# Kernel tuning notes

Hardware: AMD Instinct MI355X
Metric: run time of the kernel (lower is better)

## Reference

```python
import jax, jax.numpy as jnp
import numpy as np

S = 4096  # source_sequence_size
Q = 4096  # query_sequence_size
E = 2048  # embedding_size
D = 2048  # output_embedding_size


def setup_inputs() -> dict:
    key = jax.random.key(0)
    ks = jax.random.split(key, 9)
    s = 1.0 / np.sqrt(E)
    return {
        "key": jax.random.normal(ks[0], (S, E), jnp.float32),
        "value": jax.random.normal(ks[1], (S, E), jnp.float32),
        "query": jax.random.normal(ks[2], (Q, E), jnp.float32),
        "Wk": jax.random.normal(ks[3], (D, E), jnp.float32) * s,
        "bk": jax.random.normal(ks[4], (D,), jnp.float32) * 0.01,
        "Wq": jax.random.normal(ks[5], (D, E), jnp.float32) * s,
        "bq": jax.random.normal(ks[6], (D,), jnp.float32) * 0.01,
        "Wv": jax.random.normal(ks[7], (D, E), jnp.float32) * s,
        "bv": jax.random.normal(ks[8], (D,), jnp.float32) * 0.01,
    }


def reference(key, value, query, Wk, bk, Wq, bq, Wv, bv):
    # Linear projections (nn.Linear: x @ W.T + b)
    k = key @ Wk.T + bk      # [S, D]
    v = value @ Wv.T + bv    # [S, D]
    q = query @ Wq.T + bq    # [Q, D]
    # Per-query-token attention scores over all source tokens (schema BOTH),
    # then weighted sum over value rows -- vectorized form of the per-token
    # apply_attention_scores loop.
    scale = 1.0 / jnp.sqrt(jnp.asarray(D, q.dtype))
    scores = jax.nn.softmax(jnp.einsum("qd,sd->qs", q, k) * scale, axis=-1)  # [Q, S]
    return jnp.einsum("qs,sd->qd", scores, v)  # [Q, D]
```

## Files before the change

kernel.cpp:

```cpp
#include <hip/hip_runtime.h>

#define S_SEQ 4096
#define Q_SEQ 4096
#define E_DIM 2048
#define D_DIM 2048

typedef __bf16 bf16;
typedef __bf16 bf16x4 __attribute__((ext_vector_type(4)));
typedef __bf16 bf16x8 __attribute__((ext_vector_type(8)));
typedef float f32x4 __attribute__((ext_vector_type(4)));

__global__ __launch_bounds__(256) void cast6(
    const float* __restrict__ i0, const float* __restrict__ i1,
    const float* __restrict__ i2, const float* __restrict__ i3,
    const float* __restrict__ i4, const float* __restrict__ i5,
    bf16* __restrict__ o0, bf16* __restrict__ o1, bf16* __restrict__ o2,
    bf16* __restrict__ o3, bf16* __restrict__ o4, bf16* __restrict__ o5) {
  const float* in;
  bf16* out;
  int n4;
  switch (blockIdx.y) {
    case 0: in = i0; out = o0; n4 = (S_SEQ * E_DIM) / 4; break;
    case 1: in = i1; out = o1; n4 = (S_SEQ * E_DIM) / 4; break;
    case 2: in = i2; out = o2; n4 = (S_SEQ * E_DIM) / 4; break;
    case 3: in = i3; out = o3; n4 = (D_DIM * E_DIM) / 4; break;
    case 4: in = i4; out = o4; n4 = (D_DIM * E_DIM) / 4; break;
    default: in = i5; out = o5; n4 = (D_DIM * E_DIM) / 4; break;
  }
  int i = blockIdx.x * 256 + threadIdx.x;
  if (i < n4) {
    float4 v = reinterpret_cast<const float4*>(in)[i];
    bf16x4 o;
    o[0] = (bf16)v.x; o[1] = (bf16)v.y; o[2] = (bf16)v.z; o[3] = (bf16)v.w;
    *reinterpret_cast<bf16x4*>(out + 4 * (size_t)i) = o;
  }
}

__device__ __forceinline__ void async_copy16(const bf16* g, bf16* l) {
  __builtin_amdgcn_global_load_lds(
      (const __attribute__((address_space(1))) void*)g,
      (__attribute__((address_space(3))) void*)l, 16, 0, 0);
}

__device__ __forceinline__ void xcd_remap32(int id, int nt, int& m, int& n) {
  int xcd = id & 7;
  int lid = id >> 3;
  m = (xcd & 3) * 8 + (lid & 7);
  n = (xcd >> 2) * (nt >> 1) + (lid >> 3);
}
__device__ __forceinline__ void xcd_remap16(int id, int nt, int& m, int& n) {
  int xcd = id & 7;
  int lid = id >> 3;
  m = (xcd & 3) * 4 + (lid & 3);
  n = (xcd >> 2) * (nt >> 1) + (lid >> 2);
}

template <int EPI>
__device__ __forceinline__ void gemm_body_sb(
    const bf16* __restrict__ A, int lda,
    const bf16* __restrict__ B, int ldb,
    void* __restrict__ C, int ldc,
    const float* __restrict__ aux, float scale, int K, int mBase, int nBase) {
  __shared__ __align__(16) bf16 Als[128 * 64];
  __shared__ __align__(16) bf16 Bls[128 * 64];

  const int tid  = threadIdx.x;
  const int wave = tid >> 6;
  const int lane = tid & 63;
  const int quad = lane >> 4;
  const int lrow = lane & 15;
  const int wRow = (wave >> 1) * 64;
  const int wCol = (wave & 1) * 64;

  f32x4 acc[4][4];
#pragma unroll
  for (int i = 0; i < 4; ++i)
#pragma unroll
    for (int j = 0; j < 4; ++j) {
      f32x4 z = {0.f, 0.f, 0.f, 0.f};
      acc[i][j] = z;
    }

  for (int k0 = 0; k0 < K; k0 += 64) {
#pragma unroll
    for (int c = 0; c < 4; ++c) {
      int chunk = c * 256 + tid;
      int row = chunk >> 3;
      int kc = (chunk & 7) ^ (row & 7);
      const bf16* g = A + (size_t)(mBase + row) * lda + k0 + kc * 8;
      async_copy16(g, Als + (size_t)(c * 256 + wave * 64) * 8);
    }
#pragma unroll
    for (int c = 0; c < 4; ++c) {
      int chunk = c * 256 + tid;
      int row = chunk >> 3;
      int kc = (chunk & 7) ^ (row & 7);
      const bf16* g = B + (size_t)(nBase + row) * ldb + k0 + kc * 8;
      async_copy16(g, Bls + (size_t)(c * 256 + wave * 64) * 8);
    }
    __syncthreads();

#pragma unroll
    for (int kk = 0; kk < 2; ++kk) {
      bf16x8 af[4], bfr[4];
#pragma unroll
      for (int i = 0; i < 4; ++i) {
        int r = wRow + i * 16 + lrow;
        int slot = (kk * 4 + quad) ^ (r & 7);
        af[i] = *(const bf16x8*)(Als + (size_t)r * 64 + slot * 8);
      }
#pragma unroll
      for (int j = 0; j < 4; ++j) {
        int r = wCol + j * 16 + lrow;
        int slot = (kk * 4 + quad) ^ (r & 7);
        bfr[j] = *(const bf16x8*)(Bls + (size_t)r * 64 + slot * 8);
      }
#pragma unroll
      for (int i = 0; i < 4; ++i)
#pragma unroll
        for (int j = 0; j < 4; ++j)
          acc[i][j] = __builtin_amdgcn_mfma_f32_16x16x32_bf16(af[i], bfr[j], acc[i][j], 0, 0, 0);
    }
    __syncthreads();
  }

  float rinv[4][4];
  if (EPI == 2) {
#pragma unroll
    for (int i = 0; i < 4; ++i)
#pragma unroll
      for (int r = 0; r < 4; ++r)
        rinv[i][r] = aux[mBase + wRow + i * 16 + quad * 4 + r];
  }
#pragma unroll
  for (int j = 0; j < 4; ++j) {
    const int cn = nBase + wCol + j * 16 + lrow;
    float bj = 0.f;
    if (EPI == 0) bj = aux[cn];
#pragma unroll
    for (int i = 0; i < 4; ++i) {
      const int rbase = mBase + wRow + i * 16 + quad * 4;
#pragma unroll
      for (int r = 0; r < 4; ++r) {
        if (EPI == 0)
          ((bf16*)C)[(size_t)(rbase + r) * ldc + cn] = (bf16)(acc[i][j][r] + bj);
        else if (EPI == 1)
          ((bf16*)C)[(size_t)(rbase + r) * ldc + cn] =
              (bf16)__expf(acc[i][j][r] * scale);
        else
          ((float*)C)[(size_t)(rbase + r) * ldc + cn] = acc[i][j][r] * rinv[i][r];
      }
    }
  }
}

__device__ __forceinline__ void stage_half(const bf16* __restrict__ G, int ld,
                                           int grow0, int k0, bf16* lds,
                                           int wave, int lane) {
#pragma unroll
  for (int s = 0; s < 2; ++s) {
    int c = (wave * 2 + s) * 64 + lane;
    int row = c >> 3;
    int kc = (c & 7) ^ (row & 7);
    const bf16* g = G + (size_t)(grow0 + row) * ld + k0 + kc * 8;
    async_copy16(g, lds + (size_t)(wave * 2 + s) * 512);
  }
}

#define BARRIER __builtin_amdgcn_s_barrier()
#define LGKM0 asm volatile("s_waitcnt lgkmcnt(0)" ::: "memory")
#define VMCNT2 asm volatile("s_waitcnt vmcnt(2)" ::: "memory")
#define VMCNT0 asm volatile("s_waitcnt vmcnt(0)" ::: "memory")

#define RD_A(buf, IP)                                                         \
  _Pragma("unroll") for (int ii = 0; ii < 2; ++ii)                            \
  _Pragma("unroll") for (int kk = 0; kk < 2; ++kk)                            \
      aR[ii][kk] = *(const bf16x8*)(&Als[buf][(size_t)(wRow + ((IP)*2 + ii) * 16 + lrow) * 64 + slotk[kk] * 8]);

#define RD_B(buf, JP, dst)                                                    \
  _Pragma("unroll") for (int jj = 0; jj < 2; ++jj)                            \
  _Pragma("unroll") for (int kk = 0; kk < 2; ++kk)                            \
      dst[jj][kk] = *(const bf16x8*)(&Bls[buf][(size_t)(wCol + ((JP)*2 + jj) * 16 + lrow) * 64 + slotk[kk] * 8]);

#define MMA16(IP)                                                              \
  __builtin_amdgcn_s_setprio(1);                                               \
  _Pragma("unroll") for (int jj = 0; jj < 2; ++jj)                             \
  _Pragma("unroll") for (int ii = 0; ii < 2; ++ii)                             \
  _Pragma("unroll") for (int kk = 0; kk < 2; ++kk)                             \
      acc[(IP)*2 + ii][jj] = __builtin_amdgcn_mfma_f32_16x16x32_bf16(          \
          aR[ii][kk], b0[jj][kk], acc[(IP)*2 + ii][jj], 0, 0, 0);              \
  _Pragma("unroll") for (int jj = 0; jj < 2; ++jj)                             \
  _Pragma("unroll") for (int ii = 0; ii < 2; ++ii)                             \
  _Pragma("unroll") for (int kk = 0; kk < 2; ++kk)                             \
      acc[(IP)*2 + ii][2 + jj] = __builtin_amdgcn_mfma_f32_16x16x32_bf16(      \
          aR[ii][kk], b1[jj][kk], acc[(IP)*2 + ii][2 + jj], 0, 0, 0);          \
  __builtin_amdgcn_s_setprio(0)

template <int EPI>
__device__ __forceinline__ void gemm_body_4ph(
    const bf16* __restrict__ A, int lda,
    const bf16* __restrict__ B, int ldb,
    void* __restrict__ C, int ldc,
    const float* __restrict__ aux, float scale, int K, int mBase, int nBase,
    float* __restrict__ psum) {
  __shared__ __align__(16) bf16 Als[2][256 * 64];
  __shared__ __align__(16) bf16 Bls[2][128 * 64];

  const int tid  = threadIdx.x;
  const int wave = tid >> 6;
  const int lane = tid & 63;
  const int quad = lane >> 4;
  const int lrow = lane & 15;
  const int wRow = (wave >> 1) * 64;
  const int wCol = (wave & 1) * 64;
  const int slotk[2] = {quad ^ (lrow & 7), (4 + quad) ^ (lrow & 7)};

  f32x4 acc[4][4];
#pragma unroll
  for (int i = 0; i < 4; ++i)
#pragma unroll
    for (int j = 0; j < 4; ++j) {
      f32x4 z = {0.f, 0.f, 0.f, 0.f};
      acc[i][j] = z;
    }

  bf16x8 aR[2][2], b0[2][2], b1[2][2];

  stage_half(B, ldb, nBase, 0, &Bls[0][0], wave, lane);
  stage_half(A, lda, mBase, 0, &Als[0][0], wave, lane);
  stage_half(A, lda, mBase + 128, 0, &Als[0][128 * 64], wave, lane);
  stage_half(B, ldb, nBase, 64, &Bls[1][0], wave, lane);
  VMCNT2;
  BARRIER;

  const int NI = K >> 7;
#pragma unroll 1
  for (int i = 0; i < NI; ++i) {
    const bool nl = (i + 1 < NI);
    const int kb = i * 128;
    RD_A(0, 0);
    RD_B(0, 0, b0);
    RD_B(0, 1, b1);
    stage_half(A, lda, mBase, kb + 64, &Als[1][0], wave, lane);
    stage_half(A, lda, mBase + 128, kb + 64, &Als[1][128 * 64], wave, lane);
    BARRIER; LGKM0; MMA16(0); BARRIER;
    RD_A(0, 1);
    if (nl) {
      stage_half(B, ldb, nBase, kb + 128, &Bls[0][0], wave, lane);
      VMCNT2;
    } else {
      VMCNT0;
    }
    BARRIER; LGKM0; MMA16(1); BARRIER;
    RD_A(1, 0);
    RD_B(1, 0, b0);
    RD_B(1, 1, b1);
    if (nl) {
      stage_half(A, lda, mBase, kb + 128, &Als[0][0], wave, lane);
      stage_half(A, lda, mBase + 128, kb + 128, &Als[0][128 * 64], wave, lane);
    }
    BARRIER; LGKM0; MMA16(0); BARRIER;
    RD_A(1, 1);
    if (nl) {
      stage_half(B, ldb, nBase, kb + 192, &Bls[1][0], wave, lane);
      VMCNT2;
    }
    BARRIER; LGKM0; MMA16(1); BARRIER;
  }

  float rinv[4][4];
  if (EPI == 2) {
#pragma unroll
    for (int i = 0; i < 4; ++i)
#pragma unroll
      for (int r = 0; r < 4; ++r)
        rinv[i][r] = aux[mBase + wRow + i * 16 + quad * 4 + r];
  }
  float sp[4][4];
  if (EPI == 1) {
#pragma unroll
    for (int i = 0; i < 4; ++i)
#pragma unroll
      for (int r = 0; r < 4; ++r) sp[i][r] = 0.f;
  }
#pragma unroll
  for (int j = 0; j < 4; ++j) {
    const int cn = nBase + wCol + j * 16 + lrow;
    float bj = 0.f;
    if (EPI == 0) bj = aux[cn];
#pragma unroll
    for (int i = 0; i < 4; ++i) {
      const int rbase = mBase + wRow + i * 16 + quad * 4;
#pragma unroll
      for (int r = 0; r < 4; ++r) {
        if (EPI == 0) {
          ((bf16*)C)[(size_t)(rbase + r) * ldc + cn] = (bf16)(acc[i][j][r] + bj);
        } else if (EPI == 1) {
          bf16 eb = (bf16)__expf(acc[i][j][r] * scale);
          ((bf16*)C)[(size_t)(rbase + r) * ldc + cn] = eb;
          sp[i][r] += (float)eb;
        } else {
          ((float*)C)[(size_t)(rbase + r) * ldc + cn] = acc[i][j][r] * rinv[i][r];
        }
      }
    }
  }
  if (EPI == 1) {
#pragma unroll
    for (int i = 0; i < 4; ++i)
#pragma unroll
      for (int r = 0; r < 4; ++r) {
#pragma unroll
        for (int off = 1; off < 16; off <<= 1)
          sp[i][r] += __shfl_xor(sp[i][r], off, 64);
      }
    if (lrow == 0) {
      const int col64 = (nBase + wCol) >> 6;
#pragma unroll
      for (int i = 0; i < 4; ++i) {
        const int rbase = mBase + wRow + i * 16 + quad * 4;
#pragma unroll
        for (int r = 0; r < 4; ++r)
          psum[(size_t)(rbase + r) * 64 + col64] = sp[i][r];
      }
    }
  }
}

__global__ __launch_bounds__(512, 2) void qk_gemm(
    const bf16* __restrict__ A, const bf16* __restrict__ B,
    bf16* __restrict__ E, float scale,
    const bf16* __restrict__ v, bf16* __restrict__ vT,
    float* __restrict__ psum) {
  if (blockIdx.x >= 512) {
    __shared__ bf16 ttile[64][66];
    const int t = threadIdx.x;
    const int col = t & 63;
    const int r8 = t >> 6;
    const int base = (blockIdx.x - 512) * 4;
#pragma unroll 1
    for (int t4 = 0; t4 < 4; ++t4) {
      const int id = base + t4;
      const int c0 = (id & 31) * 64;
      const int r0 = (id >> 5) * 64;
#pragma unroll
      for (int i = 0; i < 8; ++i) {
        int rr = i * 8 + r8;
        ttile[rr][col] = v[(size_t)(r0 + rr) * D_DIM + c0 + col];
      }
      __syncthreads();
#pragma unroll
      for (int i = 0; i < 8; ++i) {
        int rr = i * 8 + r8;
        vT[(size_t)(c0 + rr) * S_SEQ + r0 + col] = ttile[col][rr];
      }
      __syncthreads();
    }
    return;
  }
  int m, n;
  xcd_remap16(blockIdx.x, 32, m, n);
  gemm_body_4ph<1>(A, D_DIM, B, D_DIM, (void*)E, S_SEQ, nullptr, scale, D_DIM,
                   m * 256, n * 128, psum);
}

__global__ __launch_bounds__(512, 2) void pv_gemm(
    const bf16* __restrict__ E, const bf16* __restrict__ vT,
    float* __restrict__ out, const float* __restrict__ inv) {
  int m, n;
  xcd_remap16(blockIdx.x, 16, m, n);
  gemm_body_4ph<2>(E, S_SEQ, vT, S_SEQ, (void*)out, D_DIM, inv, 0.f, S_SEQ,
                   m * 256, n * 128, nullptr);
}

__global__ __launch_bounds__(256, 2) void proj_gemm(
    const bf16* __restrict__ xk, const bf16* __restrict__ xq,
    const bf16* __restrict__ xv,
    const bf16* __restrict__ Wk, const bf16* __restrict__ Wq,
    const bf16* __restrict__ Wv,
    const float* __restrict__ bk, const float* __restrict__ bq,
    const float* __restrict__ bv,
    bf16* __restrict__ ok, bf16* __restrict__ oq, bf16* __restrict__ ov) {
  const bf16 *A, *W;
  const float* b;
  bf16* o;
  switch (blockIdx.z) {
    case 0: A = xk; W = Wk; b = bk; o = ok; break;
    case 1: A = xq; W = Wq; b = bq; o = oq; break;
    default: A = xv; W = Wv; b = bv; o = ov; break;
  }
  int m, n;
  xcd_remap32(blockIdx.x, 16, m, n);
  gemm_body_sb<0>(A, E_DIM, W, E_DIM, (void*)o, D_DIM, b, 0.f, E_DIM,
                  m * 128, n * 128);
}

__global__ __launch_bounds__(256) void rowsum2(
    const float* __restrict__ psum, float* __restrict__ inv) {
  const int r = blockIdx.x * 256 + threadIdx.x;
  const f32x4* p = (const f32x4*)(psum + (size_t)r * 64);
  float s = 0.f;
#pragma unroll
  for (int i = 0; i < 16; ++i) {
    f32x4 v = p[i];
    s += v[0] + v[1] + v[2] + v[3];
  }
  inv[r] = 1.0f / s;
}

extern "C" void kernel_launch(void* const* d_in, const int* in_sizes, int n_in,
                              void* d_out, int out_size, void* d_ws, size_t ws_size,
                              hipStream_t stream) {
  const float* key   = (const float*)d_in[0];
  const float* value = (const float*)d_in[1];
  const float* query = (const float*)d_in[2];
  const float* Wk = (const float*)d_in[3];
  const float* bk = (const float*)d_in[4];
  const float* Wq = (const float*)d_in[5];
  const float* bq = (const float*)d_in[6];
  const float* Wv = (const float*)d_in[7];
  const float* bv = (const float*)d_in[8];

  const size_t MB = 1ull << 20;
  char* ws = (char*)d_ws;
  bf16* key_bf   = (bf16*)(ws + 0 * MB);
  bf16* value_bf = (bf16*)(ws + 16 * MB);
  bf16* query_bf = (bf16*)(ws + 32 * MB);
  bf16* Wk_bf    = (bf16*)(ws + 48 * MB);
  bf16* Wq_bf    = (bf16*)(ws + 56 * MB);
  bf16* Wv_bf    = (bf16*)(ws + 64 * MB);
  bf16* k_bf     = (bf16*)(ws + 72 * MB);
  bf16* q_bf     = (bf16*)(ws + 88 * MB);
  bf16* v_bf     = (bf16*)(ws + 104 * MB);
  bf16* vT_bf    = (bf16*)(ws + 120 * MB);
  bf16* E        = (bf16*)(ws + 0 * MB);
  float* psum    = (float*)(ws + 34 * MB);
  float* inv     = (float*)(ws + 35 * MB);

  dim3 blk(256);
  dim3 blk512(512);

  cast6<<<dim3(8192, 6), blk, 0, stream>>>(
      key, value, query, Wk, Wq, Wv,
      key_bf, value_bf, query_bf, Wk_bf, Wq_bf, Wv_bf);

  proj_gemm<<<dim3(512, 1, 3), blk, 0, stream>>>(
      key_bf, query_bf, value_bf, Wk_bf, Wq_bf, Wv_bf, bk, bq, bv,
      k_bf, q_bf, v_bf);

  const float scale = 0.022097086912079608f;
  qk_gemm<<<dim3(1024), blk512, 0, stream>>>(q_bf, k_bf, E, scale,
                                             v_bf, vT_bf, psum);

  rowsum2<<<dim3(16), blk, 0, stream>>>(psum, inv);

  pv_gemm<<<dim3(256), blk512, 0, stream>>>(E, vT_bf, (float*)d_out, inv);
}
```

Measured before the change: 419.3 us.

## Replace 4-phase double-buffered attention GEMMs with single-buffer 256-thread GEMM

The QK and PV GEMMs drop the 512-thread, 4-phase, double-buffered LDS pipeline with priority hints. They now use a simpler 256-thread body: one LDS buffer, a 64-deep K step, and an 8x4 MFMA tile per wave. The V transpose path is adapted to 256 threads. The fp32-to-bf16 cast kernel becomes a grid-stride loop over 512 blocks instead of 8192. This cuts register pressure, barriers and launch overhead, but the global loads no longer overlap with MFMA work, which risks exposing memory latency.

```diff
diff --git a/kernel.cpp b/kernel.cpp
--- a/kernel.cpp
+++ b/kernel.cpp
@@ -27,8 +27,9 @@
     case 4: in = i4; out = o4; n4 = (D_DIM * E_DIM) / 4; break;
     default: in = i5; out = o5; n4 = (D_DIM * E_DIM) / 4; break;
   }
-  int i = blockIdx.x * 256 + threadIdx.x;
-  if (i < n4) {
+  const int stride = 512 * 256;
+#pragma unroll 2
+  for (int i = blockIdx.x * 256 + threadIdx.x; i < n4; i += stride) {
     float4 v = reinterpret_cast<const float4*>(in)[i];
     bf16x4 o;
     o[0] = (bf16)v.x; o[1] = (bf16)v.y; o[2] = (bf16)v.z; o[3] = (bf16)v.w;
@@ -124,14 +125,6 @@
     __syncthreads();
   }
 
-  float rinv[4][4];
-  if (EPI == 2) {
-#pragma unroll
-    for (int i = 0; i < 4; ++i)
-#pragma unroll
-      for (int r = 0; r < 4; ++r)
-        rinv[i][r] = aux[mBase + wRow + i * 16 + quad * 4 + r];
-  }
 #pragma unroll
   for (int j = 0; j < 4; ++j) {
     const int cn = nBase + wCol + j * 16 + lrow;
@@ -144,158 +137,105 @@
       for (int r = 0; r < 4; ++r) {
         if (EPI == 0)
           ((bf16*)C)[(size_t)(rbase + r) * ldc + cn] = (bf16)(acc[i][j][r] + bj);
-        else if (EPI == 1)
-          ((bf16*)C)[(size_t)(rbase + r) * ldc + cn] =
-              (bf16)__expf(acc[i][j][r] * scale);
-        else
-          ((float*)C)[(size_t)(rbase + r) * ldc + cn] = acc[i][j][r] * rinv[i][r];
-      }
-    }
-  }
-}
-
-__device__ __forceinline__ void stage_half(const bf16* __restrict__ G, int ld,
-                                           int grow0, int k0, bf16* lds,
-                                           int wave, int lane) {
-#pragma unroll
-  for (int s = 0; s < 2; ++s) {
-    int c = (wave * 2 + s) * 64 + lane;
-    int row = c >> 3;
-    int kc = (c & 7) ^ (row & 7);
-    const bf16* g = G + (size_t)(grow0 + row) * ld + k0 + kc * 8;
-    async_copy16(g, lds + (size_t)(wave * 2 + s) * 512);
-  }
-}
-
-#define BARRIER __builtin_amdgcn_s_barrier()
-#define LGKM0 asm volatile("s_waitcnt lgkmcnt(0)" ::: "memory")
-#define VMCNT2 asm volatile("s_waitcnt vmcnt(2)" ::: "memory")
-#define VMCNT0 asm volatile("s_waitcnt vmcnt(0)" ::: "memory")
-
-#define RD_A(buf, IP)                                                         \
-  _Pragma("unroll") for (int ii = 0; ii < 2; ++ii)                            \
-  _Pragma("unroll") for (int kk = 0; kk < 2; ++kk)                            \
-      aR[ii][kk] = *(const bf16x8*)(&Als[buf][(size_t)(wRow + ((IP)*2 + ii) * 16 + lrow) * 64 + slotk[kk] * 8]);
-
-#define RD_B(buf, JP, dst)                                                    \
-  _Pragma("unroll") for (int jj = 0; jj < 2; ++jj)                            \
-  _Pragma("unroll") for (int kk = 0; kk < 2; ++kk)                            \
-      dst[jj][kk] = *(const bf16x8*)(&Bls[buf][(size_t)(wCol + ((JP)*2 + jj) * 16 + lrow) * 64 + slotk[kk] * 8]);
-
-#define MMA16(IP)                                                              \
-  __builtin_amdgcn_s_setprio(1);                                               \
-  _Pragma("unroll") for (int jj = 0; jj < 2; ++jj)                             \
-  _Pragma("unroll") for (int ii = 0; ii < 2; ++ii)                             \
-  _Pragma("unroll") for (int kk = 0; kk < 2; ++kk)                             \
-      acc[(IP)*2 + ii][jj] = __builtin_amdgcn_mfma_f32_16x16x32_bf16(          \
-          aR[ii][kk], b0[jj][kk], acc[(IP)*2 + ii][jj], 0, 0, 0);              \
-  _Pragma("unroll") for (int jj = 0; jj < 2; ++jj)                             \
-  _Pragma("unroll") for (int ii = 0; ii < 2; ++ii)                             \
-  _Pragma("unroll") for (int kk = 0; kk < 2; ++kk)                             \
-      acc[(IP)*2 + ii][2 + jj] = __builtin_amdgcn_mfma_f32_16x16x32_bf16(      \
-          aR[ii][kk], b1[jj][kk], acc[(IP)*2 + ii][2 + jj], 0, 0, 0);          \
-  __builtin_amdgcn_s_setprio(0)
+      }
+    }
+  }
+}
 
 template <int EPI>
-__device__ __forceinline__ void gemm_body_4ph(
+__device__ __forceinline__ void gemm_body_c(
     const bf16* __restrict__ A, int lda,
     const bf16* __restrict__ B, int ldb,
     void* __restrict__ C, int ldc,
     const float* __restrict__ aux, float scale, int K, int mBase, int nBase,
     float* __restrict__ psum) {
-  __shared__ __align__(16) bf16 Als[2][256 * 64];
-  __shared__ __align__(16) bf16 Bls[2][128 * 64];
+  __shared__ __align__(16) bf16 Als[256 * 64];
+  __shared__ __align__(16) bf16 Bls[128 * 64];
 
   const int tid  = threadIdx.x;
   const int wave = tid >> 6;
   const int lane = tid & 63;
   const int quad = lane >> 4;
   const int lrow = lane & 15;
-  const int wRow = (wave >> 1) * 64;
+  const int wRow = (wave >> 1) * 128;
   const int wCol = (wave & 1) * 64;
-  const int slotk[2] = {quad ^ (lrow & 7), (4 + quad) ^ (lrow & 7)};
-
-  f32x4 acc[4][4];
-#pragma unroll
-  for (int i = 0; i < 4; ++i)
+
+  f32x4 acc[8][4];
+#pragma unroll
+  for (int i = 0; i < 8; ++i)
 #pragma unroll
     for (int j = 0; j < 4; ++j) {
       f32x4 z = {0.f, 0.f, 0.f, 0.f};
       acc[i][j] = z;
     }
 
-  bf16x8 aR[2][2], b0[2][2], b1[2][2];
-
-  stage_half(B, ldb, nBase, 0, &Bls[0][0], wave, lane);
-  stage_half(A, lda, mBase, 0, &Als[0][0], wave, lane);
-  stage_half(A, lda, mBase + 128, 0, &Als[0][128 * 64], wave, lane);
-  stage_half(B, ldb, nBase, 64, &Bls[1][0], wave, lane);
-  VMCNT2;
-  BARRIER;
-
-  const int NI = K >> 7;
-#pragma unroll 1
-  for (int i = 0; i < NI; ++i) {
-    const bool nl = (i + 1 < NI);
-    const int kb = i * 128;
-    RD_A(0, 0);
-    RD_B(0, 0, b0);
-    RD_B(0, 1, b1);
-    stage_half(A, lda, mBase, kb + 64, &Als[1][0], wave, lane);
-    stage_half(A, lda, mBase + 128, kb + 64, &Als[1][128 * 64], wave, lane);
-    BARRIER; LGKM0; MMA16(0); BARRIER;
-    RD_A(0, 1);
-    if (nl) {
-      stage_half(B, ldb, nBase, kb + 128, &Bls[0][0], wave, lane);
-      VMCNT2;
-    } else {
-      VMCNT0;
-    }
-    BARRIER; LGKM0; MMA16(1); BARRIER;
-    RD_A(1, 0);
-    RD_B(1, 0, b0);
-    RD_B(1, 1, b1);
-    if (nl) {
-      stage_half(A, lda, mBase, kb + 128, &Als[0][0], wave, lane);
-      stage_half(A, lda, mBase + 128, kb + 128, &Als[0][128 * 64], wave, lane);
-    }
-    BARRIER; LGKM0; MMA16(0); BARRIER;
-    RD_A(1, 1);
-    if (nl) {
-      stage_half(B, ldb, nBase, kb + 192, &Bls[1][0], wave, lane);
-      VMCNT2;
-    }
-    BARRIER; LGKM0; MMA16(1); BARRIER;
-  }
-
-  float rinv[4][4];
+  for (int k0 = 0; k0 < K; k0 += 64) {
+#pragma unroll
+    for (int c = 0; c < 8; ++c) {
+      int chunk = c * 256 + tid;
+      int row = chunk >> 3;
+      int kc = (chunk & 7) ^ (row & 7);
+      const bf16* g = A + (size_t)(mBase + row) * lda + k0 + kc * 8;
+      async_copy16(g, Als + (size_t)(c * 256 + wave * 64) * 8);
+    }
+#pragma unroll
+    for (int c = 0; c < 4; ++c) {
+      int chunk = c * 256 + tid;
+      int row = chunk >> 3;
+      int kc = (chunk & 7) ^ (row & 7);
+      const bf16* g = B + (size_t)(nBase + row) * ldb + k0 + kc * 8;
+      async_copy16(g, Bls + (size_t)(c * 256 + wave * 64) * 8);
+    }
+    __syncthreads();
+
+#pragma unroll
+    for (int kk = 0; kk < 2; ++kk) {
+      bf16x8 af[8], bfr[4];
+#pragma unroll
+      for (int i = 0; i < 8; ++i) {
+        int r = wRow + i * 16 + lrow;
+        int slot = (kk * 4 + quad) ^ (r & 7);
+        af[i] = *(const bf16x8*)(Als + (size_t)r * 64 + slot * 8);
+      }
+#pragma unroll
+      for (int j = 0; j < 4; ++j) {
+        int r = wCol + j * 16 + lrow;
+        int slot = (kk * 4 + quad) ^ (r & 7);
+        bfr[j] = *(const bf16x8*)(Bls + (size_t)r * 64 + slot * 8);
+      }
+#pragma unroll
+      for (int i = 0; i < 8; ++i)
+#pragma unroll
+        for (int j = 0; j < 4; ++j)
+          acc[i][j] = __builtin_amdgcn_mfma_f32_16x16x32_bf16(af[i], bfr[j], acc[i][j], 0, 0, 0);
+    }
+    __syncthreads();
+  }
+
+  float rinv[8][4];
   if (EPI == 2) {
 #pragma unroll
-    for (int i = 0; i < 4; ++i)
+    for (int i = 0; i < 8; ++i)
 #pragma unroll
       for (int r = 0; r < 4; ++r)
         rinv[i][r] = aux[mBase + wRow + i * 16 + quad * 4 + r];
   }
-  float sp[4][4];
+  float sp[8][4];
   if (EPI == 1) {
 #pragma unroll
-    for (int i = 0; i < 4; ++i)
+    for (int i = 0; i < 8; ++i)
 #pragma unroll
       for (int r = 0; r < 4; ++r) sp[i][r] = 0.f;
   }
 #pragma unroll
   for (int j = 0; j < 4; ++j) {
     const int cn = nBase + wCol + j * 16 + lrow;
-    float bj = 0.f;
-    if (EPI == 0) bj = aux[cn];
-#pragma unroll
-    for (int i = 0; i < 4; ++i) {
+#pragma unroll
+    for (int i = 0; i < 8; ++i) {
       const int rbase = mBase + wRow + i * 16 + quad * 4;
 #pragma unroll
       for (int r = 0; r < 4; ++r) {
-        if (EPI == 0) {
-          ((bf16*)C)[(size_t)(rbase + r) * ldc + cn] = (bf16)(acc[i][j][r] + bj);
-        } else if (EPI == 1) {
+        if (EPI == 1) {
           bf16 eb = (bf16)__expf(acc[i][j][r] * scale);
           ((bf16*)C)[(size_t)(rbase + r) * ldc + cn] = eb;
           sp[i][r] += (float)eb;
@@ -307,7 +247,7 @@
   }
   if (EPI == 1) {
 #pragma unroll
-    for (int i = 0; i < 4; ++i)
+    for (int i = 0; i < 8; ++i)
 #pragma unroll
       for (int r = 0; r < 4; ++r) {
 #pragma unroll
@@ -317,7 +257,7 @@
     if (lrow == 0) {
       const int col64 = (nBase + wCol) >> 6;
 #pragma unroll
-      for (int i = 0; i < 4; ++i) {
+      for (int i = 0; i < 8; ++i) {
         const int rbase = mBase + wRow + i * 16 + quad * 4;
 #pragma unroll
         for (int r = 0; r < 4; ++r)
@@ -327,7 +267,7 @@
   }
 }
 
-__global__ __launch_bounds__(512, 2) void qk_gemm(
+__global__ __launch_bounds__(256, 2) void qk_gemm(
     const bf16* __restrict__ A, const bf16* __restrict__ B,
     bf16* __restrict__ E, float scale,
     const bf16* __restrict__ v, bf16* __restrict__ vT,
@@ -336,7 +276,7 @@
     __shared__ bf16 ttile[64][66];
     const int t = threadIdx.x;
     const int col = t & 63;
-    const int r8 = t >> 6;
+    const int r4 = t >> 6;
     const int base = (blockIdx.x - 512) * 4;
 #pragma unroll 1
     for (int t4 = 0; t4 < 4; ++t4) {
@@ -344,14 +284,14 @@
       const int c0 = (id & 31) * 64;
       const int r0 = (id >> 5) * 64;
 #pragma unroll
-      for (int i = 0; i < 8; ++i) {
-        int rr = i * 8 + r8;
+      for (int i = 0; i < 16; ++i) {
+        int rr = i * 4 + r4;
         ttile[rr][col] = v[(size_t)(r0 + rr) * D_DIM + c0 + col];
       }
       __syncthreads();
 #pragma unroll
-      for (int i = 0; i < 8; ++i) {
-        int rr = i * 8 + r8;
+      for (int i = 0; i < 16; ++i) {
+        int rr = i * 4 + r4;
         vT[(size_t)(c0 + rr) * S_SEQ + r0 + col] = ttile[col][rr];
       }
       __syncthreads();
@@ -360,17 +300,17 @@
   }
   int m, n;
   xcd_remap16(blockIdx.x, 32, m, n);
-  gemm_body_4ph<1>(A, D_DIM, B, D_DIM, (void*)E, S_SEQ, nullptr, scale, D_DIM,
-                   m * 256, n * 128, psum);
-}
-
-__global__ __launch_bounds__(512, 2) void pv_gemm(
+  gemm_body_c<1>(A, D_DIM, B, D_DIM, (void*)E, S_SEQ, nullptr, scale, D_DIM,
+                 m * 256, n * 128, psum);
+}
+
+__global__ __launch_bounds__(256, 2) void pv_gemm(
     const bf16* __restrict__ E, const bf16* __restrict__ vT,
     float* __restrict__ out, const float* __restrict__ inv) {
   int m, n;
   xcd_remap16(blockIdx.x, 16, m, n);
-  gemm_body_4ph<2>(E, S_SEQ, vT, S_SEQ, (void*)out, D_DIM, inv, 0.f, S_SEQ,
-                   m * 256, n * 128, nullptr);
+  gemm_body_c<2>(E, S_SEQ, vT, S_SEQ, (void*)out, D_DIM, inv, 0.f, S_SEQ,
+                 m * 256, n * 128, nullptr);
 }
 
 __global__ __launch_bounds__(256, 2) void proj_gemm(
@@ -438,9 +378,8 @@
   float* inv     = (float*)(ws + 35 * MB);
 
   dim3 blk(256);
-  dim3 blk512(512);
-
-  cast6<<<dim3(8192, 6), blk, 0, stream>>>(
+
+  cast6<<<dim3(512, 6), blk, 0, stream>>>(
       key, value, query, Wk, Wq, Wv,
       key_bf, value_bf, query_bf, Wk_bf, Wq_bf, Wv_bf);
 
@@ -449,10 +388,10 @@
       k_bf, q_bf, v_bf);
 
   const float scale = 0.022097086912079608f;
-  qk_gemm<<<dim3(1024), blk512, 0, stream>>>(q_bf, k_bf, E, scale,
-                                             v_bf, vT_bf, psum);
+  qk_gemm<<<dim3(1024), blk, 0, stream>>>(q_bf, k_bf, E, scale,
+                                          v_bf, vT_bf, psum);
 
   rowsum2<<<dim3(16), blk, 0, stream>>>(psum, inv);
 
-  pv_gemm<<<dim3(256), blk512, 0, stream>>>(E, vT_bf, (float*)d_out, inv);
-}
+  pv_gemm<<<dim3(256), blk, 0, stream>>>(E, vT_bf, (float*)d_out, inv);
+}
```

Measured after the change: 439.9 us. 1.05x slower.

## Switch QK GEMM to simple single-buffered 256-thread kernel with larger per-wave tiles

Applied to the files above, without the earlier changes.

The QK score GEMM drops the 4-phase double-buffered 512-thread pipeline and uses a new single-buffered body with 256 threads, where each wave computes a 128x64 sub-tile (8x4 MFMA accumulators). The fused exp and partial row-sum epilogue moves into this new body, and the vT transpose blocks are adjusted for 256 threads. The 4-phase body is kept only for the PV GEMM and its EPI branching is removed. This gives up load/compute overlap in exchange for more register reuse per wave and lower LDS use, which risks exposed memory latency and higher register pressure.

```diff
diff --git a/kernel.cpp b/kernel.cpp
--- a/kernel.cpp
+++ b/kernel.cpp
@@ -124,14 +124,6 @@
     __syncthreads();
   }
 
-  float rinv[4][4];
-  if (EPI == 2) {
-#pragma unroll
-    for (int i = 0; i < 4; ++i)
-#pragma unroll
-      for (int r = 0; r < 4; ++r)
-        rinv[i][r] = aux[mBase + wRow + i * 16 + quad * 4 + r];
-  }
 #pragma unroll
   for (int j = 0; j < 4; ++j) {
     const int cn = nBase + wCol + j * 16 + lrow;
@@ -144,12 +136,116 @@
       for (int r = 0; r < 4; ++r) {
         if (EPI == 0)
           ((bf16*)C)[(size_t)(rbase + r) * ldc + cn] = (bf16)(acc[i][j][r] + bj);
-        else if (EPI == 1)
-          ((bf16*)C)[(size_t)(rbase + r) * ldc + cn] =
-              (bf16)__expf(acc[i][j][r] * scale);
-        else
-          ((float*)C)[(size_t)(rbase + r) * ldc + cn] = acc[i][j][r] * rinv[i][r];
-      }
+      }
+    }
+  }
+}
+
+template <int EPI>
+__device__ __forceinline__ void gemm_body_c(
+    const bf16* __restrict__ A, int lda,
+    const bf16* __restrict__ B, int ldb,
+    void* __restrict__ C, int ldc,
+    float scale, int K, int mBase, int nBase,
+    float* __restrict__ psum) {
+  __shared__ __align__(16) bf16 Als[256 * 64];
+  __shared__ __align__(16) bf16 Bls[128 * 64];
+
+  const int tid  = threadIdx.x;
+  const int wave = tid >> 6;
+  const int lane = tid & 63;
+  const int quad = lane >> 4;
+  const int lrow = lane & 15;
+  const int wRow = (wave >> 1) * 128;
+  const int wCol = (wave & 1) * 64;
+
+  f32x4 acc[8][4];
+#pragma unroll
+  for (int i = 0; i < 8; ++i)
+#pragma unroll
+    for (int j = 0; j < 4; ++j) {
+      f32x4 z = {0.f, 0.f, 0.f, 0.f};
+      acc[i][j] = z;
+    }
+
+  for (int k0 = 0; k0 < K; k0 += 64) {
+#pragma unroll
+    for (int c = 0; c < 8; ++c) {
+      int chunk = c * 256 + tid;
+      int row = chunk >> 3;
+      int kc = (chunk & 7) ^ (row & 7);
+      const bf16* g = A + (size_t)(mBase + row) * lda + k0 + kc * 8;
+      async_copy16(g, Als + (size_t)(c * 256 + wave * 64) * 8);
+    }
+#pragma unroll
+    for (int c = 0; c < 4; ++c) {
+      int chunk = c * 256 + tid;
+      int row = chunk >> 3;
+      int kc = (chunk & 7) ^ (row & 7);
+      const bf16* g = B + (size_t)(nBase + row) * ldb + k0 + kc * 8;
+      async_copy16(g, Bls + (size_t)(c * 256 + wave * 64) * 8);
+    }
+    __syncthreads();
+
+#pragma unroll
+    for (int kk = 0; kk < 2; ++kk) {
+      bf16x8 af[8], bfr[4];
+#pragma unroll
+      for (int i = 0; i < 8; ++i) {
+        int r = wRow + i * 16 + lrow;
+        int slot = (kk * 4 + quad) ^ (r & 7);
+        af[i] = *(const bf16x8*)(Als + (size_t)r * 64 + slot * 8);
+      }
+#pragma unroll
+      for (int j = 0; j < 4; ++j) {
+        int r = wCol + j * 16 + lrow;
+        int slot = (kk * 4 + quad) ^ (r & 7);
+        bfr[j] = *(const bf16x8*)(Bls + (size_t)r * 64 + slot * 8);
+      }
+#pragma unroll
+      for (int i = 0; i < 8; ++i)
+#pragma unroll
+        for (int j = 0; j < 4; ++j)
+          acc[i][j] = __builtin_amdgcn_mfma_f32_16x16x32_bf16(af[i], bfr[j], acc[i][j], 0, 0, 0);
+    }
+    __syncthreads();
+  }
+
+  float sp[8][4];
+#pragma unroll
+  for (int i = 0; i < 8; ++i)
+#pragma unroll
+    for (int r = 0; r < 4; ++r) sp[i][r] = 0.f;
+#pragma unroll
+  for (int j = 0; j < 4; ++j) {
+    const int cn = nBase + wCol + j * 16 + lrow;
+#pragma unroll
+    for (int i = 0; i < 8; ++i) {
+      const int rbase = mBase + wRow + i * 16 + quad * 4;
+#pragma unroll
+      for (int r = 0; r < 4; ++r) {
+        bf16 eb = (bf16)__expf(acc[i][j][r] * scale);
+        ((bf16*)C)[(size_t)(rbase + r) * ldc + cn] = eb;
+        sp[i][r] += (float)eb;
+      }
+    }
+  }
+#pragma unroll
+  for (int i = 0; i < 8; ++i)
+#pragma unroll
+    for (int r = 0; r < 4; ++r) {
+#pragma unroll
+      for (int off = 1; off < 16; off <<= 1)
+        sp[i][r] += __shfl_xor(sp[i][r], off, 64);
+    }
+  if (lrow == 0) {
+    const int col64 = (nBase + wCol) >> 6;
+#pragma unroll
+    for (int i = 0; i < 8; ++i) {
+      const int rbase = mBase + wRow + i * 16 + quad * 4;
+#pragma unroll
+      for (int r = 0; r < 4; ++r)
+        psum[(size_t)(rbase + r) * 64 + col64] = sp[i][r];
     }
   }
 }
@@ -201,8 +297,7 @@
     const bf16* __restrict__ A, int lda,
     const bf16* __restrict__ B, int ldb,
     void* __restrict__ C, int ldc,
-    const float* __restrict__ aux, float scale, int K, int mBase, int nBase,
-    float* __restrict__ psum) {
+    const float* __restrict__ aux, float scale, int K, int mBase, int nBase) {
   __shared__ __align__(16) bf16 Als[2][256 * 64];
   __shared__ __align__(16) bf16 Bls[2][128 * 64];
 
@@ -269,65 +364,25 @@
   }
 
   float rinv[4][4];
-  if (EPI == 2) {
-#pragma unroll
-    for (int i = 0; i < 4; ++i)
-#pragma unroll
-      for (int r = 0; r < 4; ++r)
-        rinv[i][r] = aux[mBase + wRow + i * 16 + quad * 4 + r];
-  }
-  float sp[4][4];
-  if (EPI == 1) {
-#pragma unroll
-    for (int i = 0; i < 4; ++i)
-#pragma unroll
-      for (int r = 0; r < 4; ++r) sp[i][r] = 0.f;
-  }
+#pragma unroll
+  for (int i = 0; i < 4; ++i)
+#pragma unroll
+    for (int r = 0; r < 4; ++r)
+      rinv[i][r] = aux[mBase + wRow + i * 16 + quad * 4 + r];
 #pragma unroll
   for (int j = 0; j < 4; ++j) {
     const int cn = nBase + wCol + j * 16 + lrow;
-    float bj = 0.f;
-    if (EPI == 0) bj = aux[cn];
 #pragma unroll
     for (int i = 0; i < 4; ++i) {
       const int rbase = mBase + wRow + i * 16 + quad * 4;
 #pragma unroll
-      for (int r = 0; r < 4; ++r) {
-        if (EPI == 0) {
-          ((bf16*)C)[(size_t)(rbase + r) * ldc + cn] = (bf16)(acc[i][j][r] + bj);
-        } else if (EPI == 1) {
-          bf16 eb = (bf16)__expf(acc[i][j][r] * scale);
-          ((bf16*)C)[(size_t)(rbase + r) * ldc + cn] = eb;
-          sp[i][r] += (float)eb;
-        } else {
-          ((float*)C)[(size_t)(rbase + r) * ldc + cn] = acc[i][j][r] * rinv[i][r];
-        }
-      }
-    }
-  }
-  if (EPI == 1) {
-#pragma unroll
-    for (int i = 0; i < 4; ++i)
-#pragma unroll
-      for (int r = 0; r < 4; ++r) {
-#pragma unroll
-        for (int off = 1; off < 16; off <<= 1)
-          sp[i][r] += __shfl_xor(sp[i][r], off, 64);
-      }
-    if (lrow == 0) {
-      const int col64 = (nBase + wCol) >> 6;
-#pragma unroll
-      for (int i = 0; i < 4; ++i) {
-        const int rbase = mBase + wRow + i * 16 + quad * 4;
-#pragma unroll
-        for (int r = 0; r < 4; ++r)
-          psum[(size_t)(rbase + r) * 64 + col64] = sp[i][r];
-      }
-    }
-  }
-}
-
-__global__ __launch_bounds__(512, 2) void qk_gemm(
+      for (int r = 0; r < 4; ++r)
+        ((float*)C)[(size_t)(rbase + r) * ldc + cn] = acc[i][j][r] * rinv[i][r];
+    }
+  }
+}
+
+__global__ __launch_bounds__(256, 2) void qk_gemm(
     const bf16* __restrict__ A, const bf16* __restrict__ B,
     bf16* __restrict__ E, float scale,
     const bf16* __restrict__ v, bf16* __restrict__ vT,
@@ -336,7 +391,7 @@
     __shared__ bf16 ttile[64][66];
     const int t = threadIdx.x;
     const int col = t & 63;
-    const int r8 = t >> 6;
+    const int r4 = t >> 6;
     const int base = (blockIdx.x - 512) * 4;
 #pragma unroll 1
     for (int t4 = 0; t4 < 4; ++t4) {
@@ -344,14 +399,14 @@
       const int c0 = (id & 31) * 64;
       const int r0 = (id >> 5) * 64;
 #pragma unroll
-      for (int i = 0; i < 8; ++i) {
-        int rr = i * 8 + r8;
+      for (int i = 0; i < 16; ++i) {
+        int rr = i * 4 + r4;
         ttile[rr][col] = v[(size_t)(r0 + rr) * D_DIM + c0 + col];
       }
       __syncthreads();
 #pragma unroll
-      for (int i = 0; i < 8; ++i) {
-        int rr = i * 8 + r8;
+      for (int i = 0; i < 16; ++i) {
+        int rr = i * 4 + r4;
         vT[(size_t)(c0 + rr) * S_SEQ + r0 + col] = ttile[col][rr];
       }
       __syncthreads();
@@ -360,8 +415,8 @@
   }
   int m, n;
   xcd_remap16(blockIdx.x, 32, m, n);
-  gemm_body_4ph<1>(A, D_DIM, B, D_DIM, (void*)E, S_SEQ, nullptr, scale, D_DIM,
-                   m * 256, n * 128, psum);
+  gemm_body_c<1>(A, D_DIM, B, D_DIM, (void*)E, S_SEQ, scale, D_DIM,
+                 m * 256, n * 128, psum);
 }
 
 __global__ __launch_bounds__(512, 2) void pv_gemm(
@@ -370,7 +425,7 @@
   int m, n;
   xcd_remap16(blockIdx.x, 16, m, n);
   gemm_body_4ph<2>(E, S_SEQ, vT, S_SEQ, (void*)out, D_DIM, inv, 0.f, S_SEQ,
-                   m * 256, n * 128, nullptr);
+                   m * 256, n * 128);
 }
 
 __global__ __launch_bounds__(256, 2) void proj_gemm(
@@ -449,8 +504,8 @@
       k_bf, q_bf, v_bf);
 
   const float scale = 0.022097086912079608f;
-  qk_gemm<<<dim3(1024), blk512, 0, stream>>>(q_bf, k_bf, E, scale,
-                                             v_bf, vT_bf, psum);
+  qk_gemm<<<dim3(1024), blk, 0, stream>>>(q_bf, k_bf, E, scale,
+                                          v_bf, vT_bf, psum);
 
   rowsum2<<<dim3(16), blk, 0, stream>>>(psum, inv);
 
```

New measurement: 419.2 us. Within noise of the previous version (-0.0%).
